# Kernel tuning notes

Measured on AMD Instinct MI355X. Metric: run time of the kernel, lower is better.

## Reference

```python
import jax, jax.numpy as jnp
import numpy as np

N = 100000   # graph nodes
E = 600000   # edges
D = 128      # feature_dim
K = 3        # candidate ops per MixedOp
EPS = 1e-5   # BatchNorm eps


def _param_stack(key, n_ops):
    kW, kb = jax.random.split(key)
    W = jax.random.normal(kW, (n_ops, K, D, D), jnp.float32) * (1.0 / np.sqrt(D))
    b = jax.random.normal(kb, (n_ops, K, D), jnp.float32) * 0.01
    g = jnp.ones((n_ops, K, D), jnp.float32)
    be = jnp.zeros((n_ops, K, D), jnp.float32)
    return W, b, g, be


def setup_inputs() -> dict:
    key = jax.random.key(0)
    ks = jax.random.split(key, 16)
    inp = {
        'src_emb': jax.random.normal(ks[0], (N, D), jnp.float32),
        'hr': jax.random.normal(ks[1], (N, D), jnp.float32),
        'edge_src': jax.random.randint(ks[2], (E,), 0, N),
        'edge_dst': jax.random.randint(ks[3], (E,), 0, N),
        'weights_zero': jax.random.uniform(ks[4], (1, K), jnp.float32),
        'weights_first': jax.random.uniform(ks[5], (3, K), jnp.float32),
        'weights_middle': jax.random.uniform(ks[6], (2, K), jnp.float32),
        'weights_last': jax.random.uniform(ks[7], (2, K), jnp.float32),
    }
    for name, k, n_ops in [('zero', ks[8], 1), ('first', ks[9], 3), ('mid', ks[10], 2), ('last', ks[11], 2)]:
        W, b, g, be = _param_stack(k, n_ops)
        inp[f'W_{name}'] = W; inp[f'b_{name}'] = b
        inp[f'g_{name}'] = g; inp[f'be_{name}'] = be
    inp['W_cat'] = jax.random.normal(ks[12], (3 * D, D), jnp.float32) * (1.0 / np.sqrt(3 * D))
    inp['b_cat'] = jax.random.normal(ks[13], (D,), jnp.float32) * 0.01
    inp['g_cat'] = jnp.ones((D,), jnp.float32)
    inp['be_cat'] = jnp.zeros((D,), jnp.float32)
    return inp


def _mean_agg(h, src, dst):
    s = jax.ops.segment_sum(h[src], dst, num_segments=N)            # [N,D]
    deg = jax.ops.segment_sum(jnp.ones((src.shape[0],), h.dtype), dst, num_segments=N)
    return s / jnp.maximum(deg, 1.0)[:, None]


def _max_agg(h, src, dst):
    m = jax.ops.segment_max(h[src], dst, num_segments=N)            # -inf for empty segs
    return jnp.where(jnp.isfinite(m), m, 0.0)


def _mixed(cands, w, W, b, g, be):
    # cands: list of K [N,D]; w:[K]; W:[K,D,D]; b/g/be:[K,D]
    x = jnp.stack(cands)                                            # [K,N,D]
    y = jnp.einsum('knd,kdf->knf', x, W) + b[:, None, :]            # Linear per candidate
    mu = jnp.mean(y, axis=1, keepdims=True)                         # BatchNorm1d (batch stats)
    var = jnp.var(y, axis=1, keepdims=True)
    y = (y - mu) * jax.lax.rsqrt(var + EPS) * g[:, None, :] + be[:, None, :]
    y = jax.nn.relu(y)
    return jnp.einsum('k,knd->nd', w, y)                            # alpha-weighted sum


def _graph_cands(h, src, dst):
    return [h, _mean_agg(h, src, dst), _max_agg(h, src, dst)]


def _cell_forward(src_emb, hr, edge_src, edge_dst,
                  weights_zero, weights_first, weights_middle, weights_last,
                  W_zero, b_zero, g_zero, be_zero,
                  W_first, b_first, g_first, be_first,
                  W_mid, b_mid, g_mid, be_mid,
                  W_last, b_last, g_last, be_last,
                  W_cat, b_cat, g_cat, be_cat):
    src, dst = edge_src, edge_dst
    # Cell_Zero: relation-composition candidates on (src_emb, hr)
    pre = [src_emb, src_emb - hr, src_emb * hr]
    h_in = _mixed(pre, weights_zero[0], W_zero[0], b_zero[0], g_zero[0], be_zero[0])
    # Cell_First (nodes=2): ops layout [(i=0,j=0),(i=1,j=0),(i=1,j=1)]
    states = [h_in]
    s0 = _mixed(_graph_cands(states[0], src, dst), weights_first[0], W_first[0], b_first[0], g_first[0], be_first[0])
    states.append(s0)
    s1 = (_mixed(_graph_cands(states[0], src, dst), weights_first[1], W_first[1], b_first[1], g_first[1], be_first[1])
          + _mixed(_graph_cands(states[1], src, dst), weights_first[2], W_first[2], b_first[2], g_first[2], be_first[2]))
    states.append(s1)
    states = states[1:]                                             # drop h_in -> len 2
    # Cell_Middle (nodes=2): one MixedOp per state
    states = [_mixed(_graph_cands(states[i], src, dst), weights_middle[i], W_mid[i], b_mid[i], g_mid[i], be_mid[i])
              for i in range(2)]
    # Cell_Last (in_nodes=2, nodes=1): one new state from both inputs; returns all 3
    s_last = (_mixed(_graph_cands(states[0], src, dst), weights_last[0], W_last[0], b_last[0], g_last[0], be_last[0])
              + _mixed(_graph_cands(states[1], src, dst), weights_last[1], W_last[1], b_last[1], g_last[1], be_last[1]))
    states = states + [s_last]                                      # len 3
    # concat -> Linear -> BN -> ReLU (dropout p=0)
    h = jnp.concatenate(states, axis=1) @ W_cat + b_cat             # [N,D]
    mu = jnp.mean(h, axis=0, keepdims=True)
    var = jnp.var(h, axis=0, keepdims=True)
    h = (h - mu) * jax.lax.rsqrt(var + EPS) * g_cat + be_cat
    return jax.nn.relu(h)


def reference(src_emb, hr, edge_src, edge_dst,
              weights_zero, weights_first, weights_middle, weights_last,
              W_zero, b_zero, g_zero, be_zero,
              W_first, b_first, g_first, be_first,
              W_mid, b_mid, g_mid, be_mid,
              W_last, b_last, g_last, be_last,
              W_cat, b_cat, g_cat, be_cat):
    return _cell_forward(src_emb, hr, edge_src, edge_dst,
                         weights_zero, weights_first, weights_middle, weights_last,
                         W_zero, b_zero, g_zero, be_zero,
                         W_first, b_first, g_first, be_first,
                         W_mid, b_mid, g_mid, be_mid,
                         W_last, b_last, g_last, be_last,
                         W_cat, b_cat, g_cat, be_cat)
```

## Files before the change

### kernel.cpp

```cpp
#include <hip/hip_runtime.h>

#define N_NODES 100000
#define N_EDGES 600000
#define NPAD    100096
#define NTILES  782
#define SCAN_B  98
#define EPS_F   1e-5f
#define GRIDG   256

typedef __bf16 bf16_t;
typedef __bf16 bf16x8 __attribute__((ext_vector_type(8)));
typedef __bf16 bf16x4 __attribute__((ext_vector_type(4)));
typedef float  f32x4  __attribute__((ext_vector_type(4)));

__global__ __launch_bounds__(256)
void init_zero_kernel(int* __restrict__ deg, float* __restrict__ stats)
{
    int i = blockIdx.x * 256 + threadIdx.x;
    if (i < N_NODES) deg[i] = 0;
    if (i < 9 * 768) stats[i] = 0.f;
}

__global__ __launch_bounds__(256)
void transpose_w_kernel(const float* __restrict__ Wz, const float* __restrict__ Wf,
                        const float* __restrict__ Wm, const float* __restrict__ Wl,
                        const float* __restrict__ Wc, bf16_t* __restrict__ wt)
{
    int idx = blockIdx.x * 256 + threadIdx.x;
    int mat = idx >> 14;
    int off = idx & 16383;
    int n = off >> 7, kk = off & 127;
    const float* src;
    if      (mat < 3)  src = Wz + mat * 16384;
    else if (mat < 12) src = Wf + (mat - 3) * 16384;
    else if (mat < 18) src = Wm + (mat - 12) * 16384;
    else if (mat < 24) src = Wl + (mat - 18) * 16384;
    else               src = Wc + (mat - 24) * 16384;
    wt[idx] = (bf16_t)src[kk * 128 + n];
}

__global__ __launch_bounds__(256)
void pre_kernel(const float* __restrict__ se, const float* __restrict__ hr,
                bf16_t* __restrict__ p0, bf16_t* __restrict__ p1, bf16_t* __restrict__ p2)
{
    long i = ((long)blockIdx.x * 256 + threadIdx.x) * 8;
    float4 a0 = *(const float4*)&se[i], a1 = *(const float4*)&se[i + 4];
    float4 b0 = *(const float4*)&hr[i], b1 = *(const float4*)&hr[i + 4];
    float av[8] = {a0.x, a0.y, a0.z, a0.w, a1.x, a1.y, a1.z, a1.w};
    float bv[8] = {b0.x, b0.y, b0.z, b0.w, b1.x, b1.y, b1.z, b1.w};
    bf16x8 o0, o1, o2;
#pragma unroll
    for (int j = 0; j < 8; ++j) {
        o0[j] = (bf16_t)av[j];
        o1[j] = (bf16_t)(av[j] - bv[j]);
        o2[j] = (bf16_t)(av[j] * bv[j]);
    }
    *(bf16x8*)&p0[i] = o0;
    *(bf16x8*)&p1[i] = o1;
    *(bf16x8*)&p2[i] = o2;
}

__global__ __launch_bounds__(256)
void deg_count_kernel(const int* __restrict__ dst, int* __restrict__ deg)
{
    int i = blockIdx.x * 256 + threadIdx.x;
    if (i < N_EDGES) atomicAdd(&deg[dst[i]], 1);
}

__global__ __launch_bounds__(256)
void scan_a_kernel(const int* __restrict__ deg, int* __restrict__ partials)
{
    __shared__ int ls[256];
    int b = blockIdx.x, t = threadIdx.x;
    int s = 0;
    for (int j = 0; j < 4; ++j) {
        int i = b * 1024 + t * 4 + j;
        if (i < N_NODES) s += deg[i];
    }
    ls[t] = s; __syncthreads();
    for (int o = 128; o > 0; o >>= 1) {
        if (t < o) ls[t] += ls[t + o];
        __syncthreads();
    }
    if (t == 0) partials[b] = ls[0];
}

__global__ void scan_b_kernel(const int* __restrict__ partials, int* __restrict__ pofs)
{
    if (threadIdx.x == 0) {
        int a = 0;
        for (int i = 0; i < SCAN_B; ++i) { pofs[i] = a; a += partials[i]; }
    }
}

__global__ __launch_bounds__(256)
void scan_c_kernel(const int* __restrict__ deg, const int* __restrict__ pofs,
                   int* __restrict__ row_ptr, int* __restrict__ cursor)
{
    __shared__ int ls[256];
    int b = blockIdx.x, t = threadIdx.x;
    int v[4], s = 0;
    for (int j = 0; j < 4; ++j) {
        int i = b * 1024 + t * 4 + j;
        v[j] = (i < N_NODES) ? deg[i] : 0;
        s += v[j];
    }
    ls[t] = s; __syncthreads();
    for (int o = 1; o < 256; o <<= 1) {
        int tv = (t >= o) ? ls[t - o] : 0;
        __syncthreads();
        ls[t] += tv;
        __syncthreads();
    }
    int excl = ls[t] - s + pofs[b];
    for (int j = 0; j < 4; ++j) {
        int i = b * 1024 + t * 4 + j;
        if (i < N_NODES) { row_ptr[i] = excl; cursor[i] = excl; excl += v[j]; }
    }
    if (b == 0 && t == 0) row_ptr[N_NODES] = N_EDGES;
}

__global__ __launch_bounds__(256)
void scatter_kernel(const int* __restrict__ src, const int* __restrict__ dst,
                    int* __restrict__ cursor, int* __restrict__ csr_src)
{
    int i = blockIdx.x * 256 + threadIdx.x;
    if (i < N_EDGES) {
        int p = atomicAdd(&cursor[dst[i]], 1);
        csr_src[p] = src[i];
    }
}

__global__ __launch_bounds__(256)
void agg_kernel(const bf16_t* __restrict__ h, const int* __restrict__ row_ptr,
                const int* __restrict__ csr_src,
                bf16_t* __restrict__ mean_o, bf16_t* __restrict__ max_o)
{
    int node = blockIdx.x * 16 + (threadIdx.x >> 4);
    int dd = (threadIdx.x & 15) * 8;
    int e0 = row_ptr[node], e1 = row_ptr[node + 1];
    float s[8], mx[8];
#pragma unroll
    for (int j = 0; j < 8; ++j) { s[j] = 0.f; mx[j] = 0.f; }
    for (int e = e0; e < e1; ++e) {
        int sc = csr_src[e];
        bf16x8 v = *(const bf16x8*)&h[(long)sc * 128 + dd];
#pragma unroll
        for (int j = 0; j < 8; ++j) {
            float f = (float)v[j];
            s[j] += f;
            mx[j] = fmaxf(mx[j], f);
        }
    }
    float inv = 1.f / fmaxf((float)(e1 - e0), 1.f);
    bf16x8 om, ox;
#pragma unroll
    for (int j = 0; j < 8; ++j) { om[j] = (bf16_t)(s[j] * inv); ox[j] = (bf16_t)mx[j]; }
    *(bf16x8*)&mean_o[(long)node * 128 + dd] = om;
    *(bf16x8*)&max_o [(long)node * 128 + dd] = ox;
}

__device__ __forceinline__ void gload_lds16(const bf16_t* g, bf16_t* l)
{
    __builtin_amdgcn_global_load_lds(
        (const __attribute__((address_space(1))) void*)g,
        (__attribute__((address_space(3))) void*)l, 16, 0, 0);
}

__device__ __forceinline__ void barrier_lgkm()
{
    asm volatile("s_waitcnt lgkmcnt(0)" ::: "memory");
    __builtin_amdgcn_s_barrier();
    asm volatile("" ::: "memory");
}

__global__ __launch_bounds__(512, 1)
void gemm_kernel(const bf16_t* __restrict__ x0, const bf16_t* __restrict__ x1,
                 const bf16_t* __restrict__ x2, const bf16_t* __restrict__ wt,
                 const float* __restrict__ bias, bf16_t* __restrict__ out,
                 float* __restrict__ partial, int mode)
{
    __shared__ __align__(16) bf16_t lds_w[2][16384];
    __shared__ __align__(16) bf16_t lds_x[2][16384];
    __shared__ float lred[512];

    const int tid  = threadIdx.x;
    const int lane = tid & 63;
    const int w8   = tid >> 6;
    const int quad = lane >> 4;
    const int t16  = lane & 15;
    const int wr = w8 >> 2, wc = w8 & 3;

    int srcoff[4], dsto[4];
#pragma unroll
    for (int i = 0; i < 4; ++i) {
        int ci = i * 512 + tid;
        int row = ci >> 4, c = ci & 15;
        srcoff[i] = row * 128 + ((c ^ (row & 15)) * 8);
        dsto[i]   = ci * 8;
    }
    auto stage = [&](const bf16_t* src, bf16_t* dst) {
#pragma unroll
        for (int i = 0; i < 4; ++i)
            gload_lds16(src + srcoff[i], dst + dsto[i]);
    };

    int s, e;
    if (mode == 0) {
        s = (int)(((long)blockIdx.x * (NTILES * 3)) / GRIDG);
        e = (int)(((long)(blockIdx.x + 1) * (NTILES * 3)) / GRIDG);
    } else {
        int st = (int)(((long)blockIdx.x * NTILES) / GRIDG);
        int et = (int)(((long)(blockIdx.x + 1) * NTILES) / GRIDG);
        s = st * 3; e = et * 3;
    }

    auto kof = [&](int w) { return (mode == 0) ? (w / NTILES) : (w % 3); };
    auto tof = [&](int w) { return (mode == 0) ? (w % NTILES) : (w / 3); };
    auto xp  = [&](int k) { return (k == 0) ? x0 : (k == 1) ? x1 : x2; };
    auto wsl = [&](int w, int k) { return (mode == 0) ? (k & 1) : (w & 1); };

    f32x4 acc[2][4];

    {
        int k0 = kof(s);
        stage(wt + (long)k0 * 16384, lds_w[wsl(s, k0)]);
        stage(xp(k0) + (long)tof(s) * 16384, lds_x[s & 1]);
    }

    for (int w = s; w < e; ++w) {
        const int ksel = kof(w), tile = tof(w);
        const bf16_t* wb = lds_w[wsl(w, ksel)];
        const bf16_t* xb = lds_x[w & 1];

        __syncthreads();

        if (w + 1 < e) {
            const int kn = kof(w + 1), tn = tof(w + 1);
            if (mode == 1 || kn != ksel)
                stage(wt + (long)kn * 16384, lds_w[wsl(w + 1, kn)]);
            stage(xp(kn) + (long)tn * 16384, lds_x[(w + 1) & 1]);
        }

        if (mode == 0 || ksel == 0) {
#pragma unroll
            for (int a = 0; a < 2; ++a)
#pragma unroll
                for (int b = 0; b < 4; ++b) acc[a][b] = (f32x4){0.f, 0.f, 0.f, 0.f};
        }

#pragma unroll
        for (int ks = 0; ks < 4; ++ks) {
            bf16x8 xf[4], wf[2];
#pragma unroll
            for (int ms = 0; ms < 4; ++ms) {
                int row = wr * 64 + ms * 16 + t16;
                int sw = (ks * 4 + quad) ^ t16;
                xf[ms] = *(const bf16x8*)&xb[row * 128 + sw * 8];
            }
#pragma unroll
            for (int ns = 0; ns < 2; ++ns) {
                int row = wc * 32 + ns * 16 + t16;
                int sw = (ks * 4 + quad) ^ t16;
                wf[ns] = *(const bf16x8*)&wb[row * 128 + sw * 8];
            }
#pragma unroll
            for (int ns = 0; ns < 2; ++ns)
#pragma unroll
                for (int ms = 0; ms < 4; ++ms)
                    acc[ns][ms] = __builtin_amdgcn_mfma_f32_16x16x32_bf16(
                        wf[ns], xf[ms], acc[ns][ms], 0, 0, 0);
        }

        if (mode == 0 || ksel == 2) {
            const float* bp = (mode == 0) ? (bias + ksel * 128) : bias;
            bf16_t* outp = (mode == 0) ? (out + (long)ksel * NPAD * 128) : out;
            const long tile_base = (long)tile * 128;

            float ss[8], sq[8];
#pragma unroll
            for (int i = 0; i < 8; ++i) { ss[i] = 0.f; sq[i] = 0.f; }

#pragma unroll
            for (int ms = 0; ms < 4; ++ms) {
                long m = tile_base + wr * 64 + ms * 16 + t16;
                if (m < N_NODES) {
#pragma unroll
                    for (int ns = 0; ns < 2; ++ns) {
                        int n0 = wc * 32 + ns * 16 + quad * 4;
                        float4 b4 = *(const float4*)&bp[n0];
                        float v0 = acc[ns][ms][0] + b4.x;
                        float v1 = acc[ns][ms][1] + b4.y;
                        float v2 = acc[ns][ms][2] + b4.z;
                        float v3 = acc[ns][ms][3] + b4.w;
                        ss[ns * 4 + 0] += v0; sq[ns * 4 + 0] += v0 * v0;
                        ss[ns * 4 + 1] += v1; sq[ns * 4 + 1] += v1 * v1;
                        ss[ns * 4 + 2] += v2; sq[ns * 4 + 2] += v2 * v2;
                        ss[ns * 4 + 3] += v3; sq[ns * 4 + 3] += v3 * v3;
                        bf16x4 ov;
                        ov[0] = (bf16_t)v0; ov[1] = (bf16_t)v1;
                        ov[2] = (bf16_t)v2; ov[3] = (bf16_t)v3;
                        *(bf16x4*)&outp[m * 128 + n0] = ov;
                    }
                }
            }

#pragma unroll
            for (int o = 1; o < 16; o <<= 1) {
#pragma unroll
                for (int i = 0; i < 8; ++i) {
                    ss[i] += __shfl_xor(ss[i], o);
                    sq[i] += __shfl_xor(sq[i], o);
                }
            }

            if (t16 == 0) {
#pragma unroll
                for (int ns = 0; ns < 2; ++ns)
#pragma unroll
                    for (int i = 0; i < 4; ++i) {
                        lred[w8 * 64 +      ns * 16 + quad * 4 + i] = ss[ns * 4 + i];
                        lred[w8 * 64 + 32 + ns * 16 + quad * 4 + i] = sq[ns * 4 + i];
                    }
            }
            barrier_lgkm();
            if (tid < 256) {
                int selo = (tid >> 7) * 32;
                int d = tid & 127;
                int wcq = d >> 5;
                int f = d & 31;
                float v = lred[wcq * 64 + selo + f] + lred[(wcq + 4) * 64 + selo + f];
                int pk = (mode == 0) ? ksel : 0;
                partial[((long)pk * NTILES + tile) * 256 + tid] = v;
            }
        }
    }
}

__global__ __launch_bounds__(256)
void reduce_stats_kernel(const float* __restrict__ partial, float* __restrict__ st)
{
    int k = blockIdx.x, j = blockIdx.y, t = threadIdx.x;
    int b0 = j * 98, b1 = (b0 + 98 < NTILES) ? b0 + 98 : NTILES;
    float s = 0.f;
    const float* p = partial + (long)k * NTILES * 256 + t;
    for (int b = b0; b < b1; ++b) s += p[(long)b * 256];
    atomicAdd(&st[k * 256 + t], s);
}

__global__ __launch_bounds__(256)
void passc_kernel(const bf16_t* __restrict__ y, const float* __restrict__ st,
                  const float* __restrict__ g, const float* __restrict__ be,
                  const float* __restrict__ w, bf16_t* __restrict__ out, int accflag)
{
    long base = ((long)blockIdx.x * 256 + threadIdx.x) * 8;
    int d0 = (int)(base & 127);
    const float invN = 1.0f / (float)N_NODES;
    float res[8];
    if (accflag) {
        bf16x8 pv = *(const bf16x8*)&out[base];
#pragma unroll
        for (int j = 0; j < 8; ++j) res[j] = (float)pv[j];
    } else {
#pragma unroll
        for (int j = 0; j < 8; ++j) res[j] = 0.f;
    }
#pragma unroll
    for (int k = 0; k < 3; ++k) {
        bf16x8 yv = *(const bf16x8*)&y[(long)k * NPAD * 128 + base];
        float wk = w[k];
#pragma unroll
        for (int j = 0; j < 8; ++j) {
            int d = d0 + j;
            float mu  = st[k * 256 + d] * invN;
            float var = st[k * 256 + 128 + d] * invN - mu * mu;
            float rs  = rsqrtf(var + EPS_F);
            float v = ((float)yv[j] - mu) * rs * g[k * 128 + d] + be[k * 128 + d];
            res[j] += wk * fmaxf(v, 0.f);
        }
    }
    bf16x8 ov;
#pragma unroll
    for (int j = 0; j < 8; ++j) ov[j] = (bf16_t)res[j];
    *(bf16x8*)&out[base] = ov;
}

__global__ __launch_bounds__(256)
void final_kernel(const bf16_t* __restrict__ h, const float* __restrict__ st,
                  const float* __restrict__ g, const float* __restrict__ be,
                  float* __restrict__ out)
{
    long base = ((long)blockIdx.x * 256 + threadIdx.x) * 8;
    int d0 = (int)(base & 127);
    const float invN = 1.0f / (float)N_NODES;
    bf16x8 hv = *(const bf16x8*)&h[base];
    float ov[8];
#pragma unroll
    for (int j = 0; j < 8; ++j) {
        int d = d0 + j;
        float mu  = st[d] * invN;
        float var = st[128 + d] * invN - mu * mu;
        float rs  = rsqrtf(var + EPS_F);
        float v = ((float)hv[j] - mu) * rs * g[d] + be[d];
        ov[j] = fmaxf(v, 0.f);
    }
    *(float4*)&out[base]     = (float4){ov[0], ov[1], ov[2], ov[3]};
    *(float4*)&out[base + 4] = (float4){ov[4], ov[5], ov[6], ov[7]};
}

extern "C" void kernel_launch(void* const* d_in, const int* in_sizes, int n_in,
                              void* d_out, int out_size, void* d_ws, size_t ws_size,
                              hipStream_t stream)
{
    const float* src_emb = (const float*)d_in[0];
    const float* hr      = (const float*)d_in[1];
    const int*   e_src   = (const int*)d_in[2];
    const int*   e_dst   = (const int*)d_in[3];
    const float* w_zero  = (const float*)d_in[4];
    const float* w_first = (const float*)d_in[5];
    const float* w_mid   = (const float*)d_in[6];
    const float* w_last  = (const float*)d_in[7];
    const float* W_zero  = (const float*)d_in[8];
    const float* b_zero  = (const float*)d_in[9];
    const float* g_zero  = (const float*)d_in[10];
    const float* be_zero = (const float*)d_in[11];
    const float* W_first = (const float*)d_in[12];
    const float* b_first = (const float*)d_in[13];
    const float* g_first = (const float*)d_in[14];
    const float* be_first= (const float*)d_in[15];
    const float* W_mid   = (const float*)d_in[16];
    const float* b_mid   = (const float*)d_in[17];
    const float* g_mid   = (const float*)d_in[18];
    const float* be_mid  = (const float*)d_in[19];
    const float* W_last  = (const float*)d_in[20];
    const float* b_last  = (const float*)d_in[21];
    const float* g_last  = (const float*)d_in[22];
    const float* be_last = (const float*)d_in[23];
    const float* W_cat   = (const float*)d_in[24];
    const float* b_cat   = (const float*)d_in[25];
    const float* g_cat   = (const float*)d_in[26];
    const float* be_cat  = (const float*)d_in[27];
    float* out = (float*)d_out;

    char* ws = (char*)d_ws;
    size_t off = 0;
    auto carve = [&](size_t bytes) -> char* {
        off = (off + 255) & ~(size_t)255;
        char* p = ws + off;
        off += bytes;
        return p;
    };

    const size_t SB = (size_t)NPAD * 128 * sizeof(bf16_t);
    bf16_t* B[8];
    for (int i = 0; i < 8; ++i) B[i] = (bf16_t*)carve(SB);
    bf16_t* ybuf = B[0];
    bf16_t* wt    = (bf16_t*)carve((size_t)27 * 16384 * 2);
    float*  stats = (float*)carve(9 * 768 * sizeof(float));
    float*  partial = (float*)carve((size_t)3 * NTILES * 256 * sizeof(float));
    int* deg    = (int*)carve((size_t)N_NODES * 4);
    int* rowp   = (int*)carve((size_t)(N_NODES + 1) * 4);
    int* cursor = (int*)carve((size_t)N_NODES * 4);
    int* csr    = (int*)carve((size_t)N_EDGES * 4);
    int* parts  = (int*)carve(SCAN_B * 4);
    int* pofs   = (int*)carve(SCAN_B * 4);

    bf16_t* wtZ  = wt;
    bf16_t* wtF0 = wt + (size_t)3  * 16384;
    bf16_t* wtF1 = wt + (size_t)6  * 16384;
    bf16_t* wtF2 = wt + (size_t)9  * 16384;
    bf16_t* wtM0 = wt + (size_t)12 * 16384;
    bf16_t* wtM1 = wt + (size_t)15 * 16384;
    bf16_t* wtL0 = wt + (size_t)18 * 16384;
    bf16_t* wtL1 = wt + (size_t)21 * 16384;
    bf16_t* wtC  = wt + (size_t)24 * 16384;

    float* st0 = stats + 0 * 768;
    float* st1 = stats + 1 * 768;
    float* st2 = stats + 2 * 768;
    float* st3 = stats + 3 * 768;
    float* st4 = stats + 4 * 768;
    float* st5 = stats + 5 * 768;
    float* st6 = stats + 6 * 768;
    float* st7 = stats + 7 * 768;
    float* st8 = stats + 8 * 768;

    const int GEL8 = (N_NODES * 128) / 2048;

    init_zero_kernel<<<dim3((N_NODES + 255) / 256), dim3(256), 0, stream>>>(deg, stats);
    transpose_w_kernel<<<dim3(1728), dim3(256), 0, stream>>>(W_zero, W_first, W_mid, W_last, W_cat, wt);
    deg_count_kernel<<<dim3((N_EDGES + 255) / 256), dim3(256), 0, stream>>>(e_dst, deg);
    scan_a_kernel<<<dim3(SCAN_B), dim3(256), 0, stream>>>(deg, parts);
    scan_b_kernel<<<dim3(1), dim3(64), 0, stream>>>(parts, pofs);
    scan_c_kernel<<<dim3(SCAN_B), dim3(256), 0, stream>>>(deg, pofs, rowp, cursor);
    scatter_kernel<<<dim3((N_EDGES + 255) / 256), dim3(256), 0, stream>>>(e_src, e_dst, cursor, csr);

    auto G = [&](const bf16_t* x0_, const bf16_t* x1_, const bf16_t* x2_,
                 const bf16_t* w_, const float* b_, bf16_t* o_, float* st_, int mode) {
        int nk = (mode == 0) ? 3 : 1;
        gemm_kernel<<<dim3(GRIDG), dim3(512), 0, stream>>>(
            x0_, x1_, x2_, w_, b_, o_, partial, mode);
        reduce_stats_kernel<<<dim3(nk, 8), dim3(256), 0, stream>>>(partial, st_);
    };
    auto C = [&](const float* g_, const float* be_, const float* w_, float* st_,
                 bf16_t* o_, int acc) {
        passc_kernel<<<dim3(GEL8), dim3(256), 0, stream>>>(ybuf, st_, g_, be_, w_, o_, acc);
    };
    auto A = [&](const bf16_t* h_, bf16_t* me_, bf16_t* mx_) {
        agg_kernel<<<dim3(N_NODES / 16), dim3(256), 0, stream>>>(h_, rowp, csr, me_, mx_);
    };

    pre_kernel<<<dim3(GEL8), dim3(256), 0, stream>>>(src_emb, hr, B[3], B[4], B[5]);
    G(B[3], B[4], B[5], wtZ, b_zero, ybuf, st0, 0);
    C(g_zero, be_zero, w_zero, st0, B[6], 0);

    A(B[6], B[3], B[4]);

    G(B[6], B[3], B[4], wtF0, b_first + 0 * 384, ybuf, st1, 0);
    C(g_first + 0 * 384, be_first + 0 * 384, w_first + 0, st1, B[5], 0);

    G(B[6], B[3], B[4], wtF1, b_first + 1 * 384, ybuf, st2, 0);
    C(g_first + 1 * 384, be_first + 1 * 384, w_first + 3, st2, B[7], 0);

    A(B[5], B[3], B[4]);

    G(B[5], B[3], B[4], wtF2, b_first + 2 * 384, ybuf, st3, 0);
    C(g_first + 2 * 384, be_first + 2 * 384, w_first + 6, st3, B[7], 1);

    G(B[5], B[3], B[4], wtM0, b_mid + 0 * 384, ybuf, st4, 0);
    C(g_mid + 0 * 384, be_mid + 0 * 384, w_mid + 0, st4, B[6], 0);

    A(B[7], B[3], B[4]);

    G(B[7], B[3], B[4], wtM1, b_mid + 1 * 384, ybuf, st5, 0);
    C(g_mid + 1 * 384, be_mid + 1 * 384, w_mid + 3, st5, B[5], 0);

    A(B[6], B[3], B[4]);
    G(B[6], B[3], B[4], wtL0, b_last + 0 * 384, ybuf, st6, 0);
    C(g_last + 0 * 384, be_last + 0 * 384, w_last + 0, st6, B[7], 0);
    A(B[5], B[3], B[4]);
    G(B[5], B[3], B[4], wtL1, b_last + 1 * 384, ybuf, st7, 0);
    C(g_last + 1 * 384, be_last + 1 * 384, w_last + 3, st7, B[7], 1);

    G(B[6], B[5], B[7], wtC, b_cat, B[0], st8, 1);
    final_kernel<<<dim3(GEL8), dim3(256), 0, stream>>>(B[0], st8, g_cat, be_cat, out);
}
```

Measured before the change: 1.285 ms.

## Fuse mixed-op GEMM, BN stats and BN apply into one persistent kernel with grid barriers

Each MixedOp's GEMM, statistics reduction and BN/ReLU/weighted-sum pass now run in a single persistent kernel. Blocks synchronise through software grid barriers on atomic counters, and the GEMM is recomputed after the statistics are known. This removes the bf16 intermediate y buffer round-trip and the separate reduce and apply kernel launches. The cost is doubling the matmul work, plus a reliance on all 256 blocks being co-resident for the spin barrier.

Measured after the change: 2.581 ms. 2.01x slower.

```diff
diff --git a/kernel.cpp b/kernel.cpp
--- a/kernel.cpp
+++ b/kernel.cpp
@@ -14,11 +14,11 @@
 typedef float  f32x4  __attribute__((ext_vector_type(4)));
 
 __global__ __launch_bounds__(256)
-void init_zero_kernel(int* __restrict__ deg, float* __restrict__ stats)
+void init_zero_kernel(int* __restrict__ deg, int* __restrict__ cnt)
 {
     int i = blockIdx.x * 256 + threadIdx.x;
     if (i < N_NODES) deg[i] = 0;
-    if (i < 9 * 768) stats[i] = 0.f;
+    if (i < 32) cnt[i] = 0;
 }
 
 __global__ __launch_bounds__(256)
@@ -174,15 +174,32 @@
     asm volatile("" ::: "memory");
 }
 
+__device__ __forceinline__ void grid_bar(int* c)
+{
+    __syncthreads();
+    if (threadIdx.x == 0) {
+        __threadfence();
+        __hip_atomic_fetch_add(c, 1, __ATOMIC_ACQ_REL, __HIP_MEMORY_SCOPE_AGENT);
+        while (__hip_atomic_load(c, __ATOMIC_ACQUIRE, __HIP_MEMORY_SCOPE_AGENT) < GRIDG)
+            __builtin_amdgcn_s_sleep(2);
+        __threadfence();
+    }
+    __syncthreads();
+    __threadfence();
+}
+
 __global__ __launch_bounds__(512, 1)
-void gemm_kernel(const bf16_t* __restrict__ x0, const bf16_t* __restrict__ x1,
-                 const bf16_t* __restrict__ x2, const bf16_t* __restrict__ wt,
-                 const float* __restrict__ bias, bf16_t* __restrict__ out,
-                 float* __restrict__ partial, int mode)
+void mixed_kernel(const bf16_t* __restrict__ x0, const bf16_t* __restrict__ x1,
+                  const bf16_t* __restrict__ x2, const bf16_t* __restrict__ wt,
+                  const float* __restrict__ bias, const float* __restrict__ gg,
+                  const float* __restrict__ be, const float* __restrict__ wmix,
+                  bf16_t* __restrict__ outb, float* __restrict__ outf,
+                  float* __restrict__ partial, float* __restrict__ tmp,
+                  int* __restrict__ cnt, int mode, int accflag)
 {
     __shared__ __align__(16) bf16_t lds_w[2][16384];
     __shared__ __align__(16) bf16_t lds_x[2][16384];
-    __shared__ float lred[512];
+    __shared__ float lsc[768];
 
     const int tid  = threadIdx.x;
     const int lane = tid & 63;
@@ -190,6 +207,8 @@
     const int quad = lane >> 4;
     const int t16  = lane & 15;
     const int wr = w8 >> 2, wc = w8 & 3;
+    const int bid = blockIdx.x;
+    const float invN = 1.0f / (float)N_NODES;
 
     int srcoff[4], dsto[4];
 #pragma unroll
@@ -204,208 +223,255 @@
         for (int i = 0; i < 4; ++i)
             gload_lds16(src + srcoff[i], dst + dsto[i]);
     };
-
-    int s, e;
-    if (mode == 0) {
-        s = (int)(((long)blockIdx.x * (NTILES * 3)) / GRIDG);
-        e = (int)(((long)(blockIdx.x + 1) * (NTILES * 3)) / GRIDG);
-    } else {
-        int st = (int)(((long)blockIdx.x * NTILES) / GRIDG);
-        int et = (int)(((long)(blockIdx.x + 1) * NTILES) / GRIDG);
-        s = st * 3; e = et * 3;
-    }
-
-    auto kof = [&](int w) { return (mode == 0) ? (w / NTILES) : (w % 3); };
-    auto tof = [&](int w) { return (mode == 0) ? (w % NTILES) : (w / 3); };
-    auto xp  = [&](int k) { return (k == 0) ? x0 : (k == 1) ? x1 : x2; };
-    auto wsl = [&](int w, int k) { return (mode == 0) ? (k & 1) : (w & 1); };
+    auto xp = [&](int c) { return (c == 0) ? x0 : (c == 1) ? x1 : x2; };
+
+    const int ts = (int)(((long)bid * NTILES) / GRIDG);
+    const int te = (int)(((long)(bid + 1) * NTILES) / GRIDG);
+    const int w0 = ts * 3, w1 = te * 3;
+    const int nk = (mode == 0) ? 3 : 1;
 
     f32x4 acc[2][4];
 
     {
-        int k0 = kof(s);
-        stage(wt + (long)k0 * 16384, lds_w[wsl(s, k0)]);
-        stage(xp(k0) + (long)tof(s) * 16384, lds_x[s & 1]);
-    }
-
-    for (int w = s; w < e; ++w) {
-        const int ksel = kof(w), tile = tof(w);
-        const bf16_t* wb = lds_w[wsl(w, ksel)];
-        const bf16_t* xb = lds_x[w & 1];
-
-        __syncthreads();
-
-        if (w + 1 < e) {
-            const int kn = kof(w + 1), tn = tof(w + 1);
-            if (mode == 1 || kn != ksel)
-                stage(wt + (long)kn * 16384, lds_w[wsl(w + 1, kn)]);
-            stage(xp(kn) + (long)tn * 16384, lds_x[(w + 1) & 1]);
+        int tile = ts, c = 0, p = 0;
+        stage(wt, lds_w[0]);
+        stage(x0 + (long)ts * 16384, lds_x[0]);
+        for (int w = w0; w < w1; ++w) {
+            __syncthreads();
+            int cn = c + 1, tn = tile;
+            if (cn == 3) { cn = 0; tn = tile + 1; }
+            if (w + 1 < w1) {
+                stage(wt + (long)cn * 16384, lds_w[p ^ 1]);
+                stage(xp(cn) + (long)tn * 16384, lds_x[p ^ 1]);
+            }
+            if (mode == 0 || c == 0) {
+#pragma unroll
+                for (int a = 0; a < 2; ++a)
+#pragma unroll
+                    for (int b = 0; b < 4; ++b) acc[a][b] = (f32x4){0.f, 0.f, 0.f, 0.f};
+            }
+#pragma unroll
+            for (int ks = 0; ks < 4; ++ks) {
+                bf16x8 xf[4], wf[2];
+#pragma unroll
+                for (int ms = 0; ms < 4; ++ms) {
+                    int row = wr * 64 + ms * 16 + t16;
+                    int sw = (ks * 4 + quad) ^ t16;
+                    xf[ms] = *(const bf16x8*)&lds_x[p][row * 128 + sw * 8];
+                }
+#pragma unroll
+                for (int ns = 0; ns < 2; ++ns) {
+                    int row = wc * 32 + ns * 16 + t16;
+                    int sw = (ks * 4 + quad) ^ t16;
+                    wf[ns] = *(const bf16x8*)&lds_w[p][row * 128 + sw * 8];
+                }
+#pragma unroll
+                for (int ns = 0; ns < 2; ++ns)
+#pragma unroll
+                    for (int ms = 0; ms < 4; ++ms)
+                        acc[ns][ms] = __builtin_amdgcn_mfma_f32_16x16x32_bf16(
+                            wf[ns], xf[ms], acc[ns][ms], 0, 0, 0);
+            }
+            if (mode == 0 || c == 2) {
+                const float* bp = bias + ((mode == 0) ? c * 128 : 0);
+                float ss[8], sq[8];
+#pragma unroll
+                for (int i = 0; i < 8; ++i) { ss[i] = 0.f; sq[i] = 0.f; }
+#pragma unroll
+                for (int ms = 0; ms < 4; ++ms) {
+                    long m = (long)tile * 128 + wr * 64 + ms * 16 + t16;
+                    if (m < N_NODES) {
+#pragma unroll
+                        for (int ns = 0; ns < 2; ++ns) {
+                            int n0 = wc * 32 + ns * 16 + quad * 4;
+                            float4 b4 = *(const float4*)&bp[n0];
+                            float v0 = acc[ns][ms][0] + b4.x;
+                            float v1 = acc[ns][ms][1] + b4.y;
+                            float v2 = acc[ns][ms][2] + b4.z;
+                            float v3 = acc[ns][ms][3] + b4.w;
+                            ss[ns * 4 + 0] += v0; sq[ns * 4 + 0] += v0 * v0;
+                            ss[ns * 4 + 1] += v1; sq[ns * 4 + 1] += v1 * v1;
+                            ss[ns * 4 + 2] += v2; sq[ns * 4 + 2] += v2 * v2;
+                            ss[ns * 4 + 3] += v3; sq[ns * 4 + 3] += v3 * v3;
+                        }
+                    }
+                }
+#pragma unroll
+                for (int o = 1; o < 16; o <<= 1) {
+#pragma unroll
+                    for (int i = 0; i < 8; ++i) {
+                        ss[i] += __shfl_xor(ss[i], o);
+                        sq[i] += __shfl_xor(sq[i], o);
+                    }
+                }
+                if (t16 == 0) {
+#pragma unroll
+                    for (int ns = 0; ns < 2; ++ns)
+#pragma unroll
+                        for (int i = 0; i < 4; ++i) {
+                            lsc[w8 * 64 +      ns * 16 + quad * 4 + i] = ss[ns * 4 + i];
+                            lsc[w8 * 64 + 32 + ns * 16 + quad * 4 + i] = sq[ns * 4 + i];
+                        }
+                }
+                barrier_lgkm();
+                if (tid < 256) {
+                    int selo = (tid >> 7) * 32;
+                    int d = tid & 127;
+                    int wcq = d >> 5, f = d & 31;
+                    float v = lsc[wcq * 64 + selo + f] + lsc[(wcq + 4) * 64 + selo + f];
+                    int slice = (mode == 0) ? c : 0;
+                    partial[((long)slice * NTILES + tile) * 256 + tid] = v;
+                }
+            }
+            p ^= 1; c = cn; tile = tn;
         }
-
-        if (mode == 0 || ksel == 0) {
-#pragma unroll
-            for (int a = 0; a < 2; ++a)
-#pragma unroll
-                for (int b = 0; b < 4; ++b) acc[a][b] = (f32x4){0.f, 0.f, 0.f, 0.f};
+    }
+
+    grid_bar(cnt + 0);
+    if (bid < nk * 16 && tid < 256) {
+        int k = bid >> 4, j = bid & 15;
+        int b0 = j * 49, b1 = (b0 + 49 < NTILES) ? b0 + 49 : NTILES;
+        float s = 0.f;
+        const float* pp = partial + (long)k * NTILES * 256 + tid;
+        for (int b = b0; b < b1; ++b) s += pp[(long)b * 256];
+        tmp[(k * 16 + j) * 256 + tid] = s;
+    }
+    grid_bar(cnt + 1);
+    if (tid < 128) {
+        for (int k = 0; k < nk; ++k) {
+            float S = 0.f, Q = 0.f;
+#pragma unroll
+            for (int j = 0; j < 16; ++j) {
+                S += tmp[(k * 16 + j) * 256 + tid];
+                Q += tmp[(k * 16 + j) * 256 + 128 + tid];
+            }
+            float mu = S * invN;
+            float var = Q * invN - mu * mu;
+            float rs = rsqrtf(var + EPS_F);
+            float gk = gg[k * 128 + tid], bek = be[k * 128 + tid];
+            float bk = bias[k * 128 + tid];
+            float wk = (mode == 0) ? wmix[k] : 1.f;
+            lsc[k * 256 + tid]       = wk * rs * gk;
+            lsc[k * 256 + 128 + tid] = wk * ((bk - mu) * rs * gk + bek);
         }
-
-#pragma unroll
-        for (int ks = 0; ks < 4; ++ks) {
-            bf16x8 xf[4], wf[2];
-#pragma unroll
-            for (int ms = 0; ms < 4; ++ms) {
-                int row = wr * 64 + ms * 16 + t16;
-                int sw = (ks * 4 + quad) ^ t16;
-                xf[ms] = *(const bf16x8*)&xb[row * 128 + sw * 8];
-            }
-#pragma unroll
-            for (int ns = 0; ns < 2; ++ns) {
-                int row = wc * 32 + ns * 16 + t16;
-                int sw = (ks * 4 + quad) ^ t16;
-                wf[ns] = *(const bf16x8*)&wb[row * 128 + sw * 8];
-            }
-#pragma unroll
-            for (int ns = 0; ns < 2; ++ns)
-#pragma unroll
-                for (int ms = 0; ms < 4; ++ms)
-                    acc[ns][ms] = __builtin_amdgcn_mfma_f32_16x16x32_bf16(
-                        wf[ns], xf[ms], acc[ns][ms], 0, 0, 0);
+    }
+    __syncthreads();
+
+    {
+        int tile = ts, c = 0, p = 0;
+        f32x4 res[2][4];
+        stage(wt, lds_w[0]);
+        stage(x0 + (long)ts * 16384, lds_x[0]);
+        for (int w = w0; w < w1; ++w) {
+            __syncthreads();
+            int cn = c + 1, tn = tile;
+            if (cn == 3) { cn = 0; tn = tile + 1; }
+            if (w + 1 < w1) {
+                stage(wt + (long)cn * 16384, lds_w[p ^ 1]);
+                stage(xp(cn) + (long)tn * 16384, lds_x[p ^ 1]);
+            }
+            if (mode == 0 || c == 0) {
+#pragma unroll
+                for (int a = 0; a < 2; ++a)
+#pragma unroll
+                    for (int b = 0; b < 4; ++b) acc[a][b] = (f32x4){0.f, 0.f, 0.f, 0.f};
+            }
+            if (mode == 0 && c == 0) {
+                if (accflag) {
+#pragma unroll
+                    for (int ns = 0; ns < 2; ++ns)
+#pragma unroll
+                        for (int ms = 0; ms < 4; ++ms) {
+                            long m = (long)tile * 128 + wr * 64 + ms * 16 + t16;
+                            int n0 = wc * 32 + ns * 16 + quad * 4;
+                            bf16x4 pv = *(const bf16x4*)&outb[m * 128 + n0];
+                            res[ns][ms] = (f32x4){(float)pv[0], (float)pv[1],
+                                                  (float)pv[2], (float)pv[3]};
+                        }
+                } else {
+#pragma unroll
+                    for (int a = 0; a < 2; ++a)
+#pragma unroll
+                        for (int b = 0; b < 4; ++b) res[a][b] = (f32x4){0.f, 0.f, 0.f, 0.f};
+                }
+            }
+#pragma unroll
+            for (int ks = 0; ks < 4; ++ks) {
+                bf16x8 xf[4], wf[2];
+#pragma unroll
+                for (int ms = 0; ms < 4; ++ms) {
+                    int row = wr * 64 + ms * 16 + t16;
+                    int sw = (ks * 4 + quad) ^ t16;
+                    xf[ms] = *(const bf16x8*)&lds_x[p][row * 128 + sw * 8];
+                }
+#pragma unroll
+                for (int ns = 0; ns < 2; ++ns) {
+                    int row = wc * 32 + ns * 16 + t16;
+                    int sw = (ks * 4 + quad) ^ t16;
+                    wf[ns] = *(const bf16x8*)&lds_w[p][row * 128 + sw * 8];
+                }
+#pragma unroll
+                for (int ns = 0; ns < 2; ++ns)
+#pragma unroll
+                    for (int ms = 0; ms < 4; ++ms)
+                        acc[ns][ms] = __builtin_amdgcn_mfma_f32_16x16x32_bf16(
+                            wf[ns], xf[ms], acc[ns][ms], 0, 0, 0);
+            }
+            if (mode == 0) {
+#pragma unroll
+                for (int ns = 0; ns < 2; ++ns) {
+                    int n0 = wc * 32 + ns * 16 + quad * 4;
+                    float4 A4 = *(const float4*)&lsc[c * 256 + n0];
+                    float4 B4 = *(const float4*)&lsc[c * 256 + 128 + n0];
+#pragma unroll
+                    for (int ms = 0; ms < 4; ++ms) {
+                        res[ns][ms][0] += fmaxf(acc[ns][ms][0] * A4.x + B4.x, 0.f);
+                        res[ns][ms][1] += fmaxf(acc[ns][ms][1] * A4.y + B4.y, 0.f);
+                        res[ns][ms][2] += fmaxf(acc[ns][ms][2] * A4.z + B4.z, 0.f);
+                        res[ns][ms][3] += fmaxf(acc[ns][ms][3] * A4.w + B4.w, 0.f);
+                    }
+                }
+                if (c == 2) {
+#pragma unroll
+                    for (int ms = 0; ms < 4; ++ms) {
+                        long m = (long)tile * 128 + wr * 64 + ms * 16 + t16;
+                        if (m < N_NODES) {
+#pragma unroll
+                            for (int ns = 0; ns < 2; ++ns) {
+                                int n0 = wc * 32 + ns * 16 + quad * 4;
+                                bf16x4 ov;
+                                ov[0] = (bf16_t)res[ns][ms][0];
+                                ov[1] = (bf16_t)res[ns][ms][1];
+                                ov[2] = (bf16_t)res[ns][ms][2];
+                                ov[3] = (bf16_t)res[ns][ms][3];
+                                *(bf16x4*)&outb[m * 128 + n0] = ov;
+                            }
+                        }
+                    }
+                }
+            } else if (c == 2) {
+#pragma unroll
+                for (int ms = 0; ms < 4; ++ms) {
+                    long m = (long)tile * 128 + wr * 64 + ms * 16 + t16;
+                    if (m < N_NODES) {
+#pragma unroll
+                        for (int ns = 0; ns < 2; ++ns) {
+                            int n0 = wc * 32 + ns * 16 + quad * 4;
+                            float4 A4 = *(const float4*)&lsc[n0];
+                            float4 B4 = *(const float4*)&lsc[128 + n0];
+                            float4 o;
+                            o.x = fmaxf(acc[ns][ms][0] * A4.x + B4.x, 0.f);
+                            o.y = fmaxf(acc[ns][ms][1] * A4.y + B4.y, 0.f);
+                            o.z = fmaxf(acc[ns][ms][2] * A4.z + B4.z, 0.f);
+                            o.w = fmaxf(acc[ns][ms][3] * A4.w + B4.w, 0.f);
+                            *(float4*)&outf[m * 128 + n0] = o;
+                        }
+                    }
+                }
+            }
+            p ^= 1; c = cn; tile = tn;
         }
-
-        if (mode == 0 || ksel == 2) {
-            const float* bp = (mode == 0) ? (bias + ksel * 128) : bias;
-            bf16_t* outp = (mode == 0) ? (out + (long)ksel * NPAD * 128) : out;
-            const long tile_base = (long)tile * 128;
-
-            float ss[8], sq[8];
-#pragma unroll
-            for (int i = 0; i < 8; ++i) { ss[i] = 0.f; sq[i] = 0.f; }
-
-#pragma unroll
-            for (int ms = 0; ms < 4; ++ms) {
-                long m = tile_base + wr * 64 + ms * 16 + t16;
-                if (m < N_NODES) {
-#pragma unroll
-                    for (int ns = 0; ns < 2; ++ns) {
-                        int n0 = wc * 32 + ns * 16 + quad * 4;
-                        float4 b4 = *(const float4*)&bp[n0];
-                        float v0 = acc[ns][ms][0] + b4.x;
-                        float v1 = acc[ns][ms][1] + b4.y;
-                        float v2 = acc[ns][ms][2] + b4.z;
-                        float v3 = acc[ns][ms][3] + b4.w;
-                        ss[ns * 4 + 0] += v0; sq[ns * 4 + 0] += v0 * v0;
-                        ss[ns * 4 + 1] += v1; sq[ns * 4 + 1] += v1 * v1;
-                        ss[ns * 4 + 2] += v2; sq[ns * 4 + 2] += v2 * v2;
-                        ss[ns * 4 + 3] += v3; sq[ns * 4 + 3] += v3 * v3;
-                        bf16x4 ov;
-                        ov[0] = (bf16_t)v0; ov[1] = (bf16_t)v1;
-                        ov[2] = (bf16_t)v2; ov[3] = (bf16_t)v3;
-                        *(bf16x4*)&outp[m * 128 + n0] = ov;
-                    }
-                }
-            }
-
-#pragma unroll
-            for (int o = 1; o < 16; o <<= 1) {
-#pragma unroll
-                for (int i = 0; i < 8; ++i) {
-                    ss[i] += __shfl_xor(ss[i], o);
-                    sq[i] += __shfl_xor(sq[i], o);
-                }
-            }
-
-            if (t16 == 0) {
-#pragma unroll
-                for (int ns = 0; ns < 2; ++ns)
-#pragma unroll
-                    for (int i = 0; i < 4; ++i) {
-                        lred[w8 * 64 +      ns * 16 + quad * 4 + i] = ss[ns * 4 + i];
-                        lred[w8 * 64 + 32 + ns * 16 + quad * 4 + i] = sq[ns * 4 + i];
-                    }
-            }
-            barrier_lgkm();
-            if (tid < 256) {
-                int selo = (tid >> 7) * 32;
-                int d = tid & 127;
-                int wcq = d >> 5;
-                int f = d & 31;
-                float v = lred[wcq * 64 + selo + f] + lred[(wcq + 4) * 64 + selo + f];
-                int pk = (mode == 0) ? ksel : 0;
-                partial[((long)pk * NTILES + tile) * 256 + tid] = v;
-            }
-        }
-    }
-}
-
-__global__ __launch_bounds__(256)
-void reduce_stats_kernel(const float* __restrict__ partial, float* __restrict__ st)
-{
-    int k = blockIdx.x, j = blockIdx.y, t = threadIdx.x;
-    int b0 = j * 98, b1 = (b0 + 98 < NTILES) ? b0 + 98 : NTILES;
-    float s = 0.f;
-    const float* p = partial + (long)k * NTILES * 256 + t;
-    for (int b = b0; b < b1; ++b) s += p[(long)b * 256];
-    atomicAdd(&st[k * 256 + t], s);
-}
-
-__global__ __launch_bounds__(256)
-void passc_kernel(const bf16_t* __restrict__ y, const float* __restrict__ st,
-                  const float* __restrict__ g, const float* __restrict__ be,
-                  const float* __restrict__ w, bf16_t* __restrict__ out, int accflag)
-{
-    long base = ((long)blockIdx.x * 256 + threadIdx.x) * 8;
-    int d0 = (int)(base & 127);
-    const float invN = 1.0f / (float)N_NODES;
-    float res[8];
-    if (accflag) {
-        bf16x8 pv = *(const bf16x8*)&out[base];
-#pragma unroll
-        for (int j = 0; j < 8; ++j) res[j] = (float)pv[j];
-    } else {
-#pragma unroll
-        for (int j = 0; j < 8; ++j) res[j] = 0.f;
-    }
-#pragma unroll
-    for (int k = 0; k < 3; ++k) {
-        bf16x8 yv = *(const bf16x8*)&y[(long)k * NPAD * 128 + base];
-        float wk = w[k];
-#pragma unroll
-        for (int j = 0; j < 8; ++j) {
-            int d = d0 + j;
-            float mu  = st[k * 256 + d] * invN;
-            float var = st[k * 256 + 128 + d] * invN - mu * mu;
-            float rs  = rsqrtf(var + EPS_F);
-            float v = ((float)yv[j] - mu) * rs * g[k * 128 + d] + be[k * 128 + d];
-            res[j] += wk * fmaxf(v, 0.f);
-        }
-    }
-    bf16x8 ov;
-#pragma unroll
-    for (int j = 0; j < 8; ++j) ov[j] = (bf16_t)res[j];
-    *(bf16x8*)&out[base] = ov;
-}
-
-__global__ __launch_bounds__(256)
-void final_kernel(const bf16_t* __restrict__ h, const float* __restrict__ st,
-                  const float* __restrict__ g, const float* __restrict__ be,
-                  float* __restrict__ out)
-{
-    long base = ((long)blockIdx.x * 256 + threadIdx.x) * 8;
-    int d0 = (int)(base & 127);
-    const float invN = 1.0f / (float)N_NODES;
-    bf16x8 hv = *(const bf16x8*)&h[base];
-    float ov[8];
-#pragma unroll
-    for (int j = 0; j < 8; ++j) {
-        int d = d0 + j;
-        float mu  = st[d] * invN;
-        float var = st[128 + d] * invN - mu * mu;
-        float rs  = rsqrtf(var + EPS_F);
-        float v = ((float)hv[j] - mu) * rs * g[d] + be[d];
-        ov[j] = fmaxf(v, 0.f);
-    }
-    *(float4*)&out[base]     = (float4){ov[0], ov[1], ov[2], ov[3]};
-    *(float4*)&out[base + 4] = (float4){ov[4], ov[5], ov[6], ov[7]};
+    }
 }
 
 extern "C" void kernel_launch(void* const* d_in, const int* in_sizes, int n_in,
@@ -454,10 +520,10 @@
     const size_t SB = (size_t)NPAD * 128 * sizeof(bf16_t);
     bf16_t* B[8];
     for (int i = 0; i < 8; ++i) B[i] = (bf16_t*)carve(SB);
-    bf16_t* ybuf = B[0];
     bf16_t* wt    = (bf16_t*)carve((size_t)27 * 16384 * 2);
-    float*  stats = (float*)carve(9 * 768 * sizeof(float));
     float*  partial = (float*)carve((size_t)3 * NTILES * 256 * sizeof(float));
+    float*  tmp   = (float*)carve((size_t)48 * 256 * sizeof(float));
+    int* cnts   = (int*)carve(32 * 4);
     int* deg    = (int*)carve((size_t)N_NODES * 4);
     int* rowp   = (int*)carve((size_t)(N_NODES + 1) * 4);
     int* cursor = (int*)carve((size_t)N_NODES * 4);
@@ -475,19 +541,9 @@
     bf16_t* wtL1 = wt + (size_t)21 * 16384;
     bf16_t* wtC  = wt + (size_t)24 * 16384;
 
-    float* st0 = stats + 0 * 768;
-    float* st1 = stats + 1 * 768;
-    float* st2 = stats + 2 * 768;
-    float* st3 = stats + 3 * 768;
-    float* st4 = stats + 4 * 768;
-    float* st5 = stats + 5 * 768;
-    float* st6 = stats + 6 * 768;
-    float* st7 = stats + 7 * 768;
-    float* st8 = stats + 8 * 768;
-
     const int GEL8 = (N_NODES * 128) / 2048;
 
-    init_zero_kernel<<<dim3((N_NODES + 255) / 256), dim3(256), 0, stream>>>(deg, stats);
+    init_zero_kernel<<<dim3((N_NODES + 255) / 256), dim3(256), 0, stream>>>(deg, cnts);
     transpose_w_kernel<<<dim3(1728), dim3(256), 0, stream>>>(W_zero, W_first, W_mid, W_last, W_cat, wt);
     deg_count_kernel<<<dim3((N_EDGES + 255) / 256), dim3(256), 0, stream>>>(e_dst, deg);
     scan_a_kernel<<<dim3(SCAN_B), dim3(256), 0, stream>>>(deg, parts);
@@ -495,53 +551,46 @@
     scan_c_kernel<<<dim3(SCAN_B), dim3(256), 0, stream>>>(deg, pofs, rowp, cursor);
     scatter_kernel<<<dim3((N_EDGES + 255) / 256), dim3(256), 0, stream>>>(e_src, e_dst, cursor, csr);
 
-    auto G = [&](const bf16_t* x0_, const bf16_t* x1_, const bf16_t* x2_,
-                 const bf16_t* w_, const float* b_, bf16_t* o_, float* st_, int mode) {
-        int nk = (mode == 0) ? 3 : 1;
-        gemm_kernel<<<dim3(GRIDG), dim3(512), 0, stream>>>(
-            x0_, x1_, x2_, w_, b_, o_, partial, mode);
-        reduce_stats_kernel<<<dim3(nk, 8), dim3(256), 0, stream>>>(partial, st_);
-    };
-    auto C = [&](const float* g_, const float* be_, const float* w_, float* st_,
-                 bf16_t* o_, int acc) {
-        passc_kernel<<<dim3(GEL8), dim3(256), 0, stream>>>(ybuf, st_, g_, be_, w_, o_, acc);
+    auto M = [&](const bf16_t* x0_, const bf16_t* x1_, const bf16_t* x2_,
+                 const bf16_t* w_, const float* b_, const float* g_, const float* be_,
+                 const float* wm_, bf16_t* ob_, float* of_, int acc_, int mode_, int id) {
+        mixed_kernel<<<dim3(GRIDG), dim3(512), 0, stream>>>(
+            x0_, x1_, x2_, w_, b_, g_, be_, wm_, ob_, of_,
+            partial, tmp, cnts + id * 2, mode_, acc_);
     };
     auto A = [&](const bf16_t* h_, bf16_t* me_, bf16_t* mx_) {
         agg_kernel<<<dim3(N_NODES / 16), dim3(256), 0, stream>>>(h_, rowp, csr, me_, mx_);
     };
 
     pre_kernel<<<dim3(GEL8), dim3(256), 0, stream>>>(src_emb, hr, B[3], B[4], B[5]);
-    G(B[3], B[4], B[5], wtZ, b_zero, ybuf, st0, 0);
-    C(g_zero, be_zero, w_zero, st0, B[6], 0);
+    M(B[3], B[4], B[5], wtZ, b_zero, g_zero, be_zero, w_zero, B[6], nullptr, 0, 0, 0);
 
     A(B[6], B[3], B[4]);
 
-    G(B[6], B[3], B[4], wtF0, b_first + 0 * 384, ybuf, st1, 0);
-    C(g_first + 0 * 384, be_first + 0 * 384, w_first + 0, st1, B[5], 0);
-
-    G(B[6], B[3], B[4], wtF1, b_first + 1 * 384, ybuf, st2, 0);
-    C(g_first + 1 * 384, be_first + 1 * 384, w_first + 3, st2, B[7], 0);
+    M(B[6], B[3], B[4], wtF0, b_first + 0, g_first + 0, be_first + 0,
+      w_first + 0, B[5], nullptr, 0, 0, 1);
+    M(B[6], B[3], B[4], wtF1, b_first + 384, g_first + 384, be_first + 384,
+      w_first + 3, B[7], nullptr, 0, 0, 2);
 
     A(B[5], B[3], B[4]);
 
-    G(B[5], B[3], B[4], wtF2, b_first + 2 * 384, ybuf, st3, 0);
-    C(g_first + 2 * 384, be_first + 2 * 384, w_first + 6, st3, B[7], 1);
-
-    G(B[5], B[3], B[4], wtM0, b_mid + 0 * 384, ybuf, st4, 0);
-    C(g_mid + 0 * 384, be_mid + 0 * 384, w_mid + 0, st4, B[6], 0);
+    M(B[5], B[3], B[4], wtF2, b_first + 768, g_first + 768, be_first + 768,
+      w_first + 6, B[7], nullptr, 1, 0, 3);
+    M(B[5], B[3], B[4], wtM0, b_mid + 0, g_mid + 0, be_mid + 0,
+      w_mid + 0, B[6], nullptr, 0, 0, 4);
 
     A(B[7], B[3], B[4]);
 
-    G(B[7], B[3], B[4], wtM1, b_mid + 1 * 384, ybuf, st5, 0);
-    C(g_mid + 1 * 384, be_mid + 1 * 384, w_mid + 3, st5, B[5], 0);
+    M(B[7], B[3], B[4], wtM1, b_mid + 384, g_mid + 384, be_mid + 384,
+      w_mid + 3, B[5], nullptr, 0, 0, 5);
 
     A(B[6], B[3], B[4]);
-    G(B[6], B[3], B[4], wtL0, b_last + 0 * 384, ybuf, st6, 0);
-    C(g_last + 0 * 384, be_last + 0 * 384, w_last + 0, st6, B[7], 0);
+    M(B[6], B[3], B[4], wtL0, b_last + 0, g_last + 0, be_last + 0,
+      w_last + 0, B[7], nullptr, 0, 0, 6);
     A(B[5], B[3], B[4]);
-    G(B[5], B[3], B[4], wtL1, b_last + 1 * 384, ybuf, st7, 0);
-    C(g_last + 1 * 384, be_last + 1 * 384, w_last + 3, st7, B[7], 1);
-
-    G(B[6], B[5], B[7], wtC, b_cat, B[0], st8, 1);
-    final_kernel<<<dim3(GEL8), dim3(256), 0, stream>>>(B[0], st8, g_cat, be_cat, out);
-}
+    M(B[5], B[3], B[4], wtL1, b_last + 384, g_last + 384, be_last + 384,
+      w_last + 3, B[7], nullptr, 1, 0, 7);
+
+    M(B[6], B[5], B[7], wtC, b_cat, g_cat, be_cat, nullptr,
+      nullptr, out, 0, 1, 8);
+}
```
